# Optimization experiments

Measured on AMD Instinct MI355X. Metric: run time of the kernel, lower is better.

The kernel has to match this reference:

```python
import jax, jax.numpy as jnp
import numpy as np

B = 128      # number of swarms
NA = 64      # agents per swarm (na)
D = 8        # input feature dim
RD = 128     # attention hidden dim r
H = 16       # output channels h (l = sqrt(h) = 4)


def setup_inputs() -> dict:
    key = jax.random.key(0)
    ks = jax.random.split(key, 16)
    x = jax.random.normal(ks[0], (B * NA, D, NA), dtype=jnp.float32)
    L = jax.random.randint(ks[1], (B * NA, D, NA), 0, 2).astype(jnp.float32)
    p = lambda k, shp: jax.random.normal(k, shp, dtype=jnp.float32)
    return {
        "x": x, "L": L,
        "Aq": p(ks[2], (RD, D)), "Ak": p(ks[3], (RD, D)), "Av": p(ks[4], (RD, D)),
        "Aq1": p(ks[5], (RD, RD)), "Ak1": p(ks[6], (RD, RD)), "Av1": p(ks[7], (RD, RD)),
        "Aq5": p(ks[8], (RD, RD)), "Ak5": p(ks[9], (RD, RD)), "Av5": p(ks[10], (RD, RD)),
        "Ao": p(ks[11], (RD, RD)), "Ao1": p(ks[12], (RD, RD)), "Ao5": p(ks[13], (H, RD)),
    }


def _attn(Xin, Aq, Ak, Av, sqrt_nn):
    # Xin: (b, f, n); Aq/Ak/Av: (r, f); sqrt_nn: (b, 1, 1)
    Q = jax.nn.sigmoid(jnp.einsum('rf,bfn->bnr', Aq, Xin))   # Q already transposed
    K = jax.nn.sigmoid(jnp.einsum('rf,bfn->brn', Ak, Xin))
    V = jax.nn.sigmoid(jnp.einsum('rf,bfn->bnr', Av, Xin))
    S = jnp.einsum('bnr,brm->bnm', Q, K) / sqrt_nn           # (b, n, n)
    A = jax.nn.softmax(S, axis=2)
    return jnp.einsum('bnm,bmr->brn', A, V)                  # o^T: (b, r, n)


def _kron_eye2(A):
    # torch.kron(A, eye(2)) per batch: (B, n, n) -> (B, 2n, 2n)
    Bq, n, _ = A.shape
    I2 = jnp.eye(2, dtype=A.dtype)
    return (A[:, :, None, :, None] * I2[None, :, None, :]).reshape(Bq, 2 * n, 2 * n)


def reference(x, L, Aq, Ak, Av, Aq1, Ak1, Av1, Aq5, Ak5, Av5, Ao, Ao1, Ao5):
    na = x.shape[2]
    Bsw = x.shape[0] // na
    num_nb = jnp.sum((L[:, 0, :] >= 1.0).astype(jnp.float32), axis=1) + 1.0
    sqrt_nn = jnp.sqrt(num_nb)[:, None, None]                # (Bx, 1, 1)

    o = _attn(x, Aq, Ak, Av, sqrt_nn)
    R = jax.nn.silu(jnp.einsum('sr,brn->bsn', Ao, o))
    o = _attn(R, Aq1, Ak1, Av1, sqrt_nn)
    R = jax.nn.silu(jnp.einsum('sr,brn->bsn', Ao1, o))
    o = _attn(R, Aq5, Ak5, Av5, sqrt_nn)
    R = jax.nn.silu(jnp.einsum('hr,brn->bhn', Ao5, o))       # (Bx, 16, na)

    blk = lambda a, b: R[:, a:b, :].sum(axis=1).reshape(Bsw, na, na)
    R11 = _kron_eye2(blk(0, 4))
    R12 = _kron_eye2(blk(4, 8))
    R21 = _kron_eye2(blk(8, 12))
    R22 = _kron_eye2(blk(12, 16))
    # block matrix [[R11, R12], [R21, R22]] -> (Bsw, 4na, 4na)
    Rfull = jnp.concatenate(
        (jnp.concatenate((R11, R21), axis=1), jnp.concatenate((R12, R22), axis=1)),
        axis=2)

    Rfull = Rfull ** 2
    Rupper = Rfull + jnp.swapaxes(Rfull, 1, 2)
    n_tot = 4 * na
    Dg = jnp.eye(n_tot, dtype=Rupper.dtype)
    Rdiag = Rupper * (1.0 - Dg)                              # diag zeroed
    Rout = Dg * Rupper                                       # keep diag only
    rowsum = jnp.sum(Rdiag, axis=2)[:, :, None]              # (Bsw, n, 1)
    return Rout + Dg * rowsum - Rdiag
```

## Files before the change

### kernel.cpp

```cpp
#include <hip/hip_runtime.h>

typedef _Float16 f16;
typedef __attribute__((ext_vector_type(8))) _Float16 h8v;
typedef __attribute__((ext_vector_type(4))) float f4v;
typedef __attribute__((ext_vector_type(16))) float f16acc;

#define OFF_WQ  0
#define OFF_WK  2048
#define OFF_WV  4096
#define OFF_AQ1 6144
#define OFF_AK1 22528
#define OFF_AV1 38912
#define OFF_AQ5 55296
#define OFF_AK5 71680
#define OFF_AV5 88064
#define OFF_AO  104448
#define OFF_AO1 120832
#define OFF_AO5 137216
#define WTS_TOTAL 139264

#define P2 136
#define P1 72

__device__ __forceinline__ f4v mfma16_(h8v a, h8v b, f4v c) {
  return __builtin_amdgcn_mfma_f32_16x16x32_f16(a, b, c, 0, 0, 0);
}
__device__ __forceinline__ f16acc mfma32_(h8v a, h8v b, f16acc c) {
  return __builtin_amdgcn_mfma_f32_32x32x16_f16(a, b, c, 0, 0, 0);
}
__device__ __forceinline__ float rcp_(float x) { return __builtin_amdgcn_rcpf(x); }
__device__ __forceinline__ float ex2_(float x) {
#if __has_builtin(__builtin_amdgcn_exp2f)
  return __builtin_amdgcn_exp2f(x);
#else
  return __expf(x * 0.6931471805599453f);
#endif
}
__device__ __forceinline__ unsigned int pk2(float a, float b) {
  __fp16 __attribute__((ext_vector_type(2))) h2 = __builtin_amdgcn_cvt_pkrtz(a, b);
  return *reinterpret_cast<unsigned int*>(&h2);
}
__device__ __forceinline__ f16acc zero16() {
  f16acc z;
  #pragma unroll
  for (int i = 0; i < 16; ++i) z[i] = 0.f;
  return z;
}

template<int ACT>
__device__ __forceinline__ unsigned long long pack4act(float a, float b, float c, float d) {
  float v[4] = {a, b, c, d};
  #pragma unroll
  for (int j = 0; j < 4; ++j) {
    float t = v[j];
    if (ACT == 0)      t = rcp_(1.0f + ex2_(t));
    else if (ACT == 1) t = t * rcp_(1.0f + ex2_(t * -1.44269504f));
    v[j] = t;
  }
  union { unsigned long long u64; unsigned int u32[2]; } u;
  u.u32[0] = pk2(v[0], v[1]);
  u.u32[1] = pk2(v[2], v[3]);
  return u.u64;
}

template<int NKK>
__device__ __forceinline__ void qkv_ph(const f16* __restrict__ Wq,
                                       const f16* __restrict__ Wk,
                                       const f16* __restrict__ Wv,
                                       const f16* __restrict__ Xt,
                                       f16* __restrict__ Qt, f16* __restrict__ Kt,
                                       f16* __restrict__ Vb, int w, int lane)
{
  const int l31 = lane & 31, lh = lane >> 5;
  const int rt = w >> 1, ct = w & 1;
  const int xbase = (ct * 32 + l31) * P2 + lh * 8;
  f16acc aq = zero16(), ak = zero16(), av = zero16();
  #pragma unroll
  for (int kk = 0; kk < NKK; ++kk) {
    h8v xf = *(const h8v*)(Xt + xbase + kk * 16);
    const int fo = (rt * NKK + kk) * 512 + lane * 8;
    h8v fq = *(const h8v*)(Wq + fo);
    h8v fk = *(const h8v*)(Wk + fo);
    h8v fv = *(const h8v*)(Wv + fo);
    aq = mfma32_(fq, xf, aq);
    ak = mfma32_(fk, xf, ak);
    av = mfma32_(xf, fv, av);
  }
  const int nrow = (ct * 32 + l31) * P2;
  const int vrow = (rt * 32 + l31) * P1 + ct * 32 + lh * 4;
  #pragma unroll
  for (int q = 0; q < 4; ++q) {
    const int rr = rt * 32 + q * 8 + lh * 4;
    *(unsigned long long*)(Qt + nrow + rr) =
        pack4act<0>(aq[4*q], aq[4*q+1], aq[4*q+2], aq[4*q+3]);
    *(unsigned long long*)(Kt + nrow + rr) =
        pack4act<0>(ak[4*q], ak[4*q+1], ak[4*q+2], ak[4*q+3]);
    *(unsigned long long*)(Vb + vrow + q * 8) =
        pack4act<0>(av[4*q], av[4*q+1], av[4*q+2], av[4*q+3]);
  }
}

__device__ __forceinline__ void softmax_ph(const f16* __restrict__ Qt,
                                           const f16* __restrict__ Kt,
                                           f16* Ps, float* __restrict__ ssum,
                                           float is2, int w, int lane)
{
  const int lrow = lane & 15, lk = lane >> 4;
  const int nst = w & 3, mh = w >> 2;
  const int n = nst * 16 + lrow;
  h8v bq[4];
  #pragma unroll
  for (int kk = 0; kk < 4; ++kk)
    bq[kk] = *(const h8v*)(Qt + n * P2 + kk * 32 + lk * 8);
  f4v acc[2];
  #pragma unroll
  for (int t = 0; t < 2; ++t) {
    const int mt = mh * 2 + t;
    acc[t] = (f4v){0.f, 0.f, 0.f, 0.f};
    #pragma unroll
    for (int kk = 0; kk < 4; ++kk) {
      h8v a = *(const h8v*)(Kt + (mt * 16 + lrow) * P2 + kk * 32 + lk * 8);
      acc[t] = mfma16_(a, bq[kk], acc[t]);
    }
  }
  float sm = 0.f;
  #pragma unroll
  for (int t = 0; t < 2; ++t)
    #pragma unroll
    for (int j = 0; j < 4; ++j) { acc[t][j] = ex2_(acc[t][j] * is2); sm += acc[t][j]; }
  sm += __shfl_xor(sm, 16);
  sm += __shfl_xor(sm, 32);
  if (lk == 0) ssum[mh * 64 + n] = sm;
  __syncthreads();
  const float inv = rcp_(ssum[n] + ssum[64 + n]);
  #pragma unroll
  for (int t = 0; t < 2; ++t) {
    const int mt = mh * 2 + t;
    union { unsigned long long u64; unsigned int u32[2]; } u;
    u.u32[0] = pk2(acc[t][0] * inv, acc[t][1] * inv);
    u.u32[1] = pk2(acc[t][2] * inv, acc[t][3] * inv);
    *(unsigned long long*)(Ps + n * P1 + mt * 16 + lk * 4) = u.u64;
  }
}

__device__ __forceinline__ void pv_ph(const f16* __restrict__ Vb,
                                      const f16* __restrict__ Ps,
                                      f16* __restrict__ Ot, int w, int lane)
{
  const int l31 = lane & 31, lh = lane >> 5;
  const int rt = w >> 1, ct = w & 1;
  f16acc acc = zero16();
  #pragma unroll
  for (int kk = 0; kk < 4; ++kk) {
    h8v a = *(const h8v*)(Vb + (rt * 32 + l31) * P1 + kk * 16 + lh * 8);
    h8v b = *(const h8v*)(Ps + (ct * 32 + l31) * P1 + kk * 16 + lh * 8);
    acc = mfma32_(a, b, acc);
  }
  const int nrow = (ct * 32 + l31) * P2;
  #pragma unroll
  for (int q = 0; q < 4; ++q)
    *(unsigned long long*)(Ot + nrow + rt * 32 + q * 8 + lh * 4) =
        pack4act<2>(acc[4*q], acc[4*q+1], acc[4*q+2], acc[4*q+3]);
}

__device__ __forceinline__ void ao_ph(const f16* __restrict__ Ao,
                                      const f16* __restrict__ Ot,
                                      f16* __restrict__ Rt, int w, int lane)
{
  const int l31 = lane & 31, lh = lane >> 5;
  const int st = w >> 1, ct = w & 1;
  f16acc acc = zero16();
  #pragma unroll
  for (int kk = 0; kk < 8; ++kk) {
    h8v a = *(const h8v*)(Ao + (st * 8 + kk) * 512 + lane * 8);
    h8v b = *(const h8v*)(Ot + (ct * 32 + l31) * P2 + kk * 16 + lh * 8);
    acc = mfma32_(a, b, acc);
  }
  const int nrow = (ct * 32 + l31) * P2;
  #pragma unroll
  for (int q = 0; q < 4; ++q)
    *(unsigned long long*)(Rt + nrow + st * 32 + q * 8 + lh * 4) =
        pack4act<1>(acc[4*q], acc[4*q+1], acc[4*q+2], acc[4*q+3]);
}

__device__ __forceinline__ void final_ph(const f16* __restrict__ Ao5g,
                                         const f16* __restrict__ Ot,
                                         float* __restrict__ rch_b, int w, int lane)
{
  const int lrow = lane & 15, lk = lane >> 4;
  h8v a[4];
  #pragma unroll
  for (int kk = 0; kk < 4; ++kk)
    a[kk] = *(const h8v*)(Ao5g + lrow * 128 + kk * 32 + lk * 8);
  const int n = 16 * w + lrow;
  f4v acc = {0.f, 0.f, 0.f, 0.f};
  #pragma unroll
  for (int kk = 0; kk < 4; ++kk) {
    h8v b = *(const h8v*)(Ot + n * P2 + kk * 32 + lk * 8);
    acc = mfma16_(a[kk], b, acc);
  }
  #pragma unroll
  for (int j = 0; j < 4; ++j) {
    float v = acc[j];
    v = v * rcp_(1.0f + ex2_(v * -1.44269504f));
    rch_b[(lk * 4 + j) * 64 + n] = v;
  }
}

__global__ __launch_bounds__(512, 4)
void swarm_attn_mfma(const float* __restrict__ x, const float* __restrict__ L,
                     const f16* __restrict__ wts, float* __restrict__ rch)
{
  __shared__ f16 Xt[64 * P2];
  __shared__ f16 Qt[64 * P2];
  __shared__ f16 Kt[64 * P2];
  __shared__ f16 Vb[128 * P1];
  __shared__ float ssum[2 * 64];
  f16* Ps = Xt;

  const int b = blockIdx.x;
  const int tid = threadIdx.x;
  const int w = tid >> 6, lane = tid & 63;

  {
    const int n = tid >> 3, c = tid & 7;
    unsigned int val = 0;
    if (c < 4) {
      const float a  = x[(size_t)b * 512 + (2 * c) * 64 + n];
      const float bb = x[(size_t)b * 512 + (2 * c + 1) * 64 + n];
      val = pk2(a, bb);
    }
    *(unsigned int*)(Xt + n * P2 + 2 * c) = val;
  }
  const float lv = L[(size_t)b * 512 + lane];
  const unsigned long long msk = __ballot(lv >= 1.0f);
  const float is2 = __frsqrt_rn((float)(__popcll(msk) + 1)) * 1.44269504f;
  __syncthreads();

  qkv_ph<1>(wts + OFF_WQ, wts + OFF_WK, wts + OFF_WV, Xt, Qt, Kt, Vb, w, lane);
  __syncthreads();
  softmax_ph(Qt, Kt, Ps, ssum, is2, w, lane);
  __syncthreads();
  pv_ph(Vb, Ps, Qt, w, lane);
  __syncthreads();
  ao_ph(wts + OFF_AO, Qt, Xt, w, lane);
  __syncthreads();

  qkv_ph<8>(wts + OFF_AQ1, wts + OFF_AK1, wts + OFF_AV1, Xt, Qt, Kt, Vb, w, lane);
  __syncthreads();
  softmax_ph(Qt, Kt, Ps, ssum, is2, w, lane);
  __syncthreads();
  pv_ph(Vb, Ps, Qt, w, lane);
  __syncthreads();
  ao_ph(wts + OFF_AO1, Qt, Xt, w, lane);
  __syncthreads();

  qkv_ph<8>(wts + OFF_AQ5, wts + OFF_AK5, wts + OFF_AV5, Xt, Qt, Kt, Vb, w, lane);
  __syncthreads();
  softmax_ph(Qt, Kt, Ps, ssum, is2, w, lane);
  __syncthreads();
  pv_ph(Vb, Ps, Qt, w, lane);
  __syncthreads();
  if (w < 4) final_ph(wts + OFF_AO5, Qt, rch + (size_t)b * 1024, w, lane);
}

__global__ void conv_wts(const float* Aq, const float* Ak, const float* Av,
                         const float* Aq1, const float* Ak1, const float* Av1,
                         const float* Aq5, const float* Ak5, const float* Av5,
                         const float* Ao, const float* Ao1, const float* Ao5,
                         f16* wts)
{
  const float SCL = -1.44269504088896f;
  const int t = blockIdx.x * 256 + threadIdx.x;
  if (t >= WTS_TOTAL) return;
  float v;
  if (t < 6144) {
    const int m = t >> 11, idx = t & 2047;
    const int fi = idx >> 9, rem = idx & 511, lane = rem >> 3, j = rem & 7;
    const int r = fi * 32 + (lane & 31), k = (lane >> 5) * 8 + j;
    const float* W = (m == 0) ? Aq : (m == 1) ? Ak : Av;
    v = (k < 8) ? W[r * 8 + k] * SCL : 0.f;
  } else if (t < 137216) {
    const int m = (t - 6144) >> 14, idx = (t - 6144) & 16383;
    const int fi = idx >> 9, rem = idx & 511, lane = rem >> 3, j = rem & 7;
    const int rt = fi >> 3, kk = fi & 7;
    const int r = rt * 32 + (lane & 31), k = kk * 16 + (lane >> 5) * 8 + j;
    const float* W = (m == 0) ? Aq1 : (m == 1) ? Ak1 : (m == 2) ? Av1 :
                     (m == 3) ? Aq5 : (m == 4) ? Ak5 : (m == 5) ? Av5 :
                     (m == 6) ? Ao : Ao1;
    v = W[r * 128 + k];
    if (m < 6) v *= SCL;
  } else {
    v = Ao5[t - 137216];
  }
  wts[t] = (f16)v;
}

#define ASTR 65
__global__ __launch_bounds__(256, 1)
void reduce_kernel(const float* __restrict__ rch, float* __restrict__ Mw,
                   float* __restrict__ rsw, float* __restrict__ csw)
{
  __shared__ float Msh[4 * 64 * ASTR];
  const int s = blockIdx.x, t = threadIdx.x;
  for (int e = t; e < 16384; e += 256) {
    const int j = e & 63, i = (e >> 6) & 63, g = e >> 12;
    const float* p = rch + ((size_t)s * 64 + i) * 1024 + (4 * g) * 64 + j;
    const float v = p[0] + p[64] + p[128] + p[192];
    Msh[(g * 64 + i) * ASTR + j] = v;
    Mw[(size_t)s * 16384 + e] = v;
  }
  __syncthreads();
  const int g = t >> 6, i = t & 63;
  float r2 = 0.f, c2 = 0.f;
  for (int j = 0; j < 64; ++j) {
    const float a = Msh[(g * 64 + i) * ASTR + j];
    const float bb = Msh[(g * 64 + j) * ASTR + i];
    r2 = fmaf(a, a, r2);
    c2 = fmaf(bb, bb, c2);
  }
  rsw[s * 256 + g * 64 + i] = r2;
  csw[s * 256 + g * 64 + i] = c2;
}

__global__ __launch_bounds__(256, 1)
void expand_kernel(const float* __restrict__ Mw, const float* __restrict__ rsw,
                   const float* __restrict__ csw, float* __restrict__ out)
{
  const size_t e = ((size_t)blockIdx.x * 256 + threadIdx.x) * 4;
  const int s = (int)(e >> 16);
  const int rem = (int)(e & 65535);
  const int u = rem >> 8, v0 = rem & 255;
  const int ub = u >> 7, ii = (u & 127) >> 1, p = u & 1;
  const float* Ms = Mw + (size_t)s * 16384;
  float4 o;
  float* po = &o.x;
  #pragma unroll
  for (int c = 0; c < 4; ++c) {
    const int v = v0 + c;
    const int vb = v >> 7, jj = (v & 127) >> 1, q = v & 1;
    float val = 0.f;
    if (u == v) {
      val = rsw[s * 256 + (2 * ub) * 64 + ii] + rsw[s * 256 + (2 * ub + 1) * 64 + ii]
          + csw[s * 256 + ub * 64 + ii] + csw[s * 256 + (2 + ub) * 64 + ii];
    } else if (p == q) {
      const int g = 2 * ub + vb, gp = 2 * vb + ub;
      const float a = Ms[g * 4096 + ii * 64 + jj];
      const float bb = Ms[gp * 4096 + jj * 64 + ii];
      val = -(a * a + bb * bb);
    }
    po[c] = val;
  }
  *(float4*)(out + e) = o;
}

extern "C" void kernel_launch(void* const* d_in, const int* in_sizes, int n_in,
                              void* d_out, int out_size, void* d_ws, size_t ws_size,
                              hipStream_t stream)
{
  const float* x   = (const float*)d_in[0];
  const float* L   = (const float*)d_in[1];
  const float* Aq  = (const float*)d_in[2];
  const float* Ak  = (const float*)d_in[3];
  const float* Av  = (const float*)d_in[4];
  const float* Aq1 = (const float*)d_in[5];
  const float* Ak1 = (const float*)d_in[6];
  const float* Av1 = (const float*)d_in[7];
  const float* Aq5 = (const float*)d_in[8];
  const float* Ak5 = (const float*)d_in[9];
  const float* Av5 = (const float*)d_in[10];
  const float* Ao  = (const float*)d_in[11];
  const float* Ao1 = (const float*)d_in[12];
  const float* Ao5 = (const float*)d_in[13];

  f16* wts = (f16*)d_ws;
  float* Mw  = (float*)((char*)d_ws + (size_t)WTS_TOTAL * 2);
  float* rsw = Mw + (size_t)128 * 16384;
  float* csw = rsw + 128 * 256;
  float* rch = (float*)d_out;

  conv_wts<<<(WTS_TOTAL + 255) / 256, 256, 0, stream>>>(Aq, Ak, Av, Aq1, Ak1, Av1,
                                                        Aq5, Ak5, Av5, Ao, Ao1, Ao5, wts);
  swarm_attn_mfma<<<8192, 512, 0, stream>>>(x, L, wts, rch);
  reduce_kernel<<<128, 256, 0, stream>>>(rch, Mw, rsw, csw);
  expand_kernel<<<8192, 256, 0, stream>>>(Mw, rsw, csw, (float*)d_out);
}
```

Before: 320.7 us.

## Fuse softmax with PV in registers and fold block sums into final phase

Merges the softmax and P·V phases so each wave computes full softmax rows in registers and feeds the fp16 probabilities straight into 16x16x16 MFMAs. This removes the shared-memory P buffer, the cross-wave row-sum exchange and one barrier per layer. The final phase now sums the four channels of each block in registers and writes the reduced matrix directly, so the reduce kernel only reloads it and the 1024-float intermediate round trip through global memory is gone. Launch bounds drop from 4 to 2 blocks per CU, which gives more registers but may lower occupancy. Each wave also recomputes the full 64-wide score row, doubling QK MFMA work per wave.

```diff
diff --git a/kernel.cpp b/kernel.cpp
--- a/kernel.cpp
+++ b/kernel.cpp
@@ -1,6 +1,7 @@
 #include <hip/hip_runtime.h>
 
 typedef _Float16 f16;
+typedef __attribute__((ext_vector_type(4))) _Float16 h4v;
 typedef __attribute__((ext_vector_type(8))) _Float16 h8v;
 typedef __attribute__((ext_vector_type(4))) float f4v;
 typedef __attribute__((ext_vector_type(16))) float f16acc;
@@ -25,6 +26,9 @@
 __device__ __forceinline__ f4v mfma16_(h8v a, h8v b, f4v c) {
   return __builtin_amdgcn_mfma_f32_16x16x32_f16(a, b, c, 0, 0, 0);
 }
+__device__ __forceinline__ f4v mfma16k16_(h4v a, h4v b, f4v c) {
+  return __builtin_amdgcn_mfma_f32_16x16x16f16(a, b, c, 0, 0, 0);
+}
 __device__ __forceinline__ f16acc mfma32_(h8v a, h8v b, f16acc c) {
   return __builtin_amdgcn_mfma_f32_32x32x16_f16(a, b, c, 0, 0, 0);
 }
@@ -100,67 +104,57 @@
   }
 }
 
-__device__ __forceinline__ void softmax_ph(const f16* __restrict__ Qt,
-                                           const f16* __restrict__ Kt,
-                                           f16* Ps, float* __restrict__ ssum,
-                                           float is2, int w, int lane)
-{
-  const int lrow = lane & 15, lk = lane >> 4;
-  const int nst = w & 3, mh = w >> 2;
-  const int n = nst * 16 + lrow;
+__device__ __forceinline__ void smpv_ph(const f16* __restrict__ Qt,
+                                        const f16* __restrict__ Kt,
+                                        const f16* __restrict__ Vb,
+                                        f16* __restrict__ Ot,
+                                        float is2, int w, int lane)
+{
+  const int l15 = lane & 15, lk = lane >> 4;
+  const int nst = w & 3, rh = w >> 2;
+  const int n = nst * 16 + l15;
   h8v bq[4];
   #pragma unroll
   for (int kk = 0; kk < 4; ++kk)
     bq[kk] = *(const h8v*)(Qt + n * P2 + kk * 32 + lk * 8);
-  f4v acc[2];
-  #pragma unroll
-  for (int t = 0; t < 2; ++t) {
-    const int mt = mh * 2 + t;
-    acc[t] = (f4v){0.f, 0.f, 0.f, 0.f};
+  f4v acc[4];
+  #pragma unroll
+  for (int mt = 0; mt < 4; ++mt) {
+    acc[mt] = (f4v){0.f, 0.f, 0.f, 0.f};
     #pragma unroll
     for (int kk = 0; kk < 4; ++kk) {
-      h8v a = *(const h8v*)(Kt + (mt * 16 + lrow) * P2 + kk * 32 + lk * 8);
-      acc[t] = mfma16_(a, bq[kk], acc[t]);
+      h8v a = *(const h8v*)(Kt + (mt * 16 + l15) * P2 + kk * 32 + lk * 8);
+      acc[mt] = mfma16_(a, bq[kk], acc[mt]);
     }
   }
   float sm = 0.f;
   #pragma unroll
-  for (int t = 0; t < 2; ++t)
+  for (int mt = 0; mt < 4; ++mt)
     #pragma unroll
-    for (int j = 0; j < 4; ++j) { acc[t][j] = ex2_(acc[t][j] * is2); sm += acc[t][j]; }
+    for (int j = 0; j < 4; ++j) { acc[mt][j] = ex2_(acc[mt][j] * is2); sm += acc[mt][j]; }
   sm += __shfl_xor(sm, 16);
   sm += __shfl_xor(sm, 32);
-  if (lk == 0) ssum[mh * 64 + n] = sm;
-  __syncthreads();
-  const float inv = rcp_(ssum[n] + ssum[64 + n]);
-  #pragma unroll
-  for (int t = 0; t < 2; ++t) {
-    const int mt = mh * 2 + t;
-    union { unsigned long long u64; unsigned int u32[2]; } u;
-    u.u32[0] = pk2(acc[t][0] * inv, acc[t][1] * inv);
-    u.u32[1] = pk2(acc[t][2] * inv, acc[t][3] * inv);
-    *(unsigned long long*)(Ps + n * P1 + mt * 16 + lk * 4) = u.u64;
-  }
-}
-
-__device__ __forceinline__ void pv_ph(const f16* __restrict__ Vb,
-                                      const f16* __restrict__ Ps,
-                                      f16* __restrict__ Ot, int w, int lane)
-{
-  const int l31 = lane & 31, lh = lane >> 5;
-  const int rt = w >> 1, ct = w & 1;
-  f16acc acc = zero16();
-  #pragma unroll
-  for (int kk = 0; kk < 4; ++kk) {
-    h8v a = *(const h8v*)(Vb + (rt * 32 + l31) * P1 + kk * 16 + lh * 8);
-    h8v b = *(const h8v*)(Ps + (ct * 32 + l31) * P1 + kk * 16 + lh * 8);
-    acc = mfma32_(a, b, acc);
-  }
-  const int nrow = (ct * 32 + l31) * P2;
-  #pragma unroll
-  for (int q = 0; q < 4; ++q)
-    *(unsigned long long*)(Ot + nrow + rt * 32 + q * 8 + lh * 4) =
-        pack4act<2>(acc[4*q], acc[4*q+1], acc[4*q+2], acc[4*q+3]);
+  const float inv = rcp_(sm);
+  h4v p[4];
+  #pragma unroll
+  for (int mt = 0; mt < 4; ++mt) {
+    union { unsigned long long u64; unsigned int u32[2]; h4v h; } u;
+    u.u32[0] = pk2(acc[mt][0] * inv, acc[mt][1] * inv);
+    u.u32[1] = pk2(acc[mt][2] * inv, acc[mt][3] * inv);
+    p[mt] = u.h;
+  }
+  #pragma unroll
+  for (int rt2 = 0; rt2 < 4; ++rt2) {
+    const int rtile = rh * 4 + rt2;
+    f4v o = (f4v){0.f, 0.f, 0.f, 0.f};
+    #pragma unroll
+    for (int mt = 0; mt < 4; ++mt) {
+      h4v vf = *(const h4v*)(Vb + (rtile * 16 + l15) * P1 + mt * 16 + lk * 4);
+      o = mfma16k16_(vf, p[mt], o);
+    }
+    *(unsigned long long*)(Ot + n * P2 + rtile * 16 + lk * 4) =
+        pack4act<2>(o[0], o[1], o[2], o[3]);
+  }
 }
 
 __device__ __forceinline__ void ao_ph(const f16* __restrict__ Ao,
@@ -185,7 +179,7 @@
 
 __device__ __forceinline__ void final_ph(const f16* __restrict__ Ao5g,
                                          const f16* __restrict__ Ot,
-                                         float* __restrict__ rch_b, int w, int lane)
+                                         float* __restrict__ Mw, int b, int w, int lane)
 {
   const int lrow = lane & 15, lk = lane >> 4;
   h8v a[4];
@@ -196,27 +190,27 @@
   f4v acc = {0.f, 0.f, 0.f, 0.f};
   #pragma unroll
   for (int kk = 0; kk < 4; ++kk) {
-    h8v b = *(const h8v*)(Ot + n * P2 + kk * 32 + lk * 8);
-    acc = mfma16_(a[kk], b, acc);
-  }
+    h8v bb = *(const h8v*)(Ot + n * P2 + kk * 32 + lk * 8);
+    acc = mfma16_(a[kk], bb, acc);
+  }
+  float msum = 0.f;
   #pragma unroll
   for (int j = 0; j < 4; ++j) {
     float v = acc[j];
     v = v * rcp_(1.0f + ex2_(v * -1.44269504f));
-    rch_b[(lk * 4 + j) * 64 + n] = v;
-  }
-}
-
-__global__ __launch_bounds__(512, 4)
+    msum += v;
+  }
+  Mw[(size_t)(b >> 6) * 16384 + lk * 4096 + (b & 63) * 64 + n] = msum;
+}
+
+__global__ __launch_bounds__(512, 2)
 void swarm_attn_mfma(const float* __restrict__ x, const float* __restrict__ L,
-                     const f16* __restrict__ wts, float* __restrict__ rch)
-{
-  __shared__ f16 Xt[64 * P2];
-  __shared__ f16 Qt[64 * P2];
-  __shared__ f16 Kt[64 * P2];
+                     const f16* __restrict__ wts, float* __restrict__ Mw)
+{
+  __shared__ f16 B0[64 * P2];
+  __shared__ f16 B1[64 * P2];
+  __shared__ f16 B2[64 * P2];
   __shared__ f16 Vb[128 * P1];
-  __shared__ float ssum[2 * 64];
-  f16* Ps = Xt;
 
   const int b = blockIdx.x;
   const int tid = threadIdx.x;
@@ -230,38 +224,32 @@
       const float bb = x[(size_t)b * 512 + (2 * c + 1) * 64 + n];
       val = pk2(a, bb);
     }
-    *(unsigned int*)(Xt + n * P2 + 2 * c) = val;
+    *(unsigned int*)(B0 + n * P2 + 2 * c) = val;
   }
   const float lv = L[(size_t)b * 512 + lane];
   const unsigned long long msk = __ballot(lv >= 1.0f);
   const float is2 = __frsqrt_rn((float)(__popcll(msk) + 1)) * 1.44269504f;
   __syncthreads();
 
-  qkv_ph<1>(wts + OFF_WQ, wts + OFF_WK, wts + OFF_WV, Xt, Qt, Kt, Vb, w, lane);
-  __syncthreads();
-  softmax_ph(Qt, Kt, Ps, ssum, is2, w, lane);
-  __syncthreads();
-  pv_ph(Vb, Ps, Qt, w, lane);
-  __syncthreads();
-  ao_ph(wts + OFF_AO, Qt, Xt, w, lane);
-  __syncthreads();
-
-  qkv_ph<8>(wts + OFF_AQ1, wts + OFF_AK1, wts + OFF_AV1, Xt, Qt, Kt, Vb, w, lane);
-  __syncthreads();
-  softmax_ph(Qt, Kt, Ps, ssum, is2, w, lane);
-  __syncthreads();
-  pv_ph(Vb, Ps, Qt, w, lane);
-  __syncthreads();
-  ao_ph(wts + OFF_AO1, Qt, Xt, w, lane);
-  __syncthreads();
-
-  qkv_ph<8>(wts + OFF_AQ5, wts + OFF_AK5, wts + OFF_AV5, Xt, Qt, Kt, Vb, w, lane);
-  __syncthreads();
-  softmax_ph(Qt, Kt, Ps, ssum, is2, w, lane);
-  __syncthreads();
-  pv_ph(Vb, Ps, Qt, w, lane);
-  __syncthreads();
-  if (w < 4) final_ph(wts + OFF_AO5, Qt, rch + (size_t)b * 1024, w, lane);
+  qkv_ph<1>(wts + OFF_WQ, wts + OFF_WK, wts + OFF_WV, B0, B1, B2, Vb, w, lane);
+  __syncthreads();
+  smpv_ph(B1, B2, Vb, B0, is2, w, lane);
+  __syncthreads();
+  ao_ph(wts + OFF_AO, B0, B1, w, lane);
+  __syncthreads();
+
+  qkv_ph<8>(wts + OFF_AQ1, wts + OFF_AK1, wts + OFF_AV1, B1, B0, B2, Vb, w, lane);
+  __syncthreads();
+  smpv_ph(B0, B2, Vb, B1, is2, w, lane);
+  __syncthreads();
+  ao_ph(wts + OFF_AO1, B1, B0, w, lane);
+  __syncthreads();
+
+  qkv_ph<8>(wts + OFF_AQ5, wts + OFF_AK5, wts + OFF_AV5, B0, B1, B2, Vb, w, lane);
+  __syncthreads();
+  smpv_ph(B1, B2, Vb, B0, is2, w, lane);
+  __syncthreads();
+  if (w < 4) final_ph(wts + OFF_AO5, B0, Mw, b, w, lane);
 }
 
 __global__ void conv_wts(const float* Aq, const float* Ak, const float* Av,
@@ -298,17 +286,14 @@
 
 #define ASTR 65
 __global__ __launch_bounds__(256, 1)
-void reduce_kernel(const float* __restrict__ rch, float* __restrict__ Mw,
+void reduce_kernel(const float* __restrict__ Mw,
                    float* __restrict__ rsw, float* __restrict__ csw)
 {
   __shared__ float Msh[4 * 64 * ASTR];
   const int s = blockIdx.x, t = threadIdx.x;
   for (int e = t; e < 16384; e += 256) {
     const int j = e & 63, i = (e >> 6) & 63, g = e >> 12;
-    const float* p = rch + ((size_t)s * 64 + i) * 1024 + (4 * g) * 64 + j;
-    const float v = p[0] + p[64] + p[128] + p[192];
-    Msh[(g * 64 + i) * ASTR + j] = v;
-    Mw[(size_t)s * 16384 + e] = v;
+    Msh[(g * 64 + i) * ASTR + j] = Mw[(size_t)s * 16384 + e];
   }
   __syncthreads();
   const int g = t >> 6, i = t & 63;
@@ -377,11 +362,10 @@
   float* Mw  = (float*)((char*)d_ws + (size_t)WTS_TOTAL * 2);
   float* rsw = Mw + (size_t)128 * 16384;
   float* csw = rsw + 128 * 256;
-  float* rch = (float*)d_out;
 
   conv_wts<<<(WTS_TOTAL + 255) / 256, 256, 0, stream>>>(Aq, Ak, Av, Aq1, Ak1, Av1,
                                                         Aq5, Ak5, Av5, Ao, Ao1, Ao5, wts);
-  swarm_attn_mfma<<<8192, 512, 0, stream>>>(x, L, wts, rch);
-  reduce_kernel<<<128, 256, 0, stream>>>(rch, Mw, rsw, csw);
+  swarm_attn_mfma<<<8192, 512, 0, stream>>>(x, L, wts, Mw);
+  reduce_kernel<<<128, 256, 0, stream>>>(Mw, rsw, csw);
   expand_kernel<<<8192, 256, 0, stream>>>(Mw, rsw, csw, (float*)d_out);
 }
```

New measurement: 337.8 us. 5.3% more time.
